# Kernel tuning notes

Measured on AMD Instinct MI355X. Metric: run time of the kernel, lower is better.

The kernel has to match this reference:

```python
import jax, jax.numpy as jnp
import numpy as np

N, D, C = 32768, 1024, 256
GAMMA = 1e-4


def setup_inputs() -> dict:
    key = jax.random.key(0)
    kx, kw = jax.random.split(key)
    X = jax.random.normal(kx, (N, D), dtype=jnp.float32)
    # lcls linear params: weight [C, D], bias [C] (torch nn.Linear layout)
    W = jax.random.normal(kw, (C, D), dtype=jnp.float32) * (1.0 / np.sqrt(D))
    b = jnp.zeros((C,), dtype=jnp.float32)
    return {"X": X, "W": W, "b": b}


def reference(X, W, b):
    # P = softmax(X @ W.T + b) over cluster dim C
    P = jax.nn.softmax(X @ W.T + b, axis=-1)            # [N, C]
    # Reorder P @ P.T @ X -> P @ (P.T @ X): avoids the O(N^2) affinity matrix
    PtX = jnp.einsum('nc,nd->cd', P, X)                  # [C, D]
    return X + GAMMA * (P @ PtX)                         # [N, D]
```

## Files before the change

### kernel.cpp

```cpp
#include <hip/hip_runtime.h>
#include <hip/hip_bf16.h>
#include <stdint.h>

#define N_TOK 32768
#define DIM   1024
#define NC    256
#define GAMMA_F 1e-4f

typedef unsigned short u16;
typedef __attribute__((ext_vector_type(8))) short bf16x8;
typedef __attribute__((ext_vector_type(4))) float f32x4;

__device__ __forceinline__ u16 f2b(float f) {
  union { float f; uint32_t u; } c; c.f = f;
  uint32_t u = c.u;
  return (u16)((u + 0x7FFFu + ((u >> 16) & 1u)) >> 16);
}

__device__ __forceinline__ void gll16(const void* g, void* l) {
  __builtin_amdgcn_global_load_lds(
      (const __attribute__((address_space(1))) unsigned int*)g,
      (__attribute__((address_space(3))) unsigned int*)l, 16, 0, 0);
}


__global__ __launch_bounds__(256) void k0_transpose(const float* __restrict__ X,
                                                    u16* __restrict__ TX) {
  __shared__ u16 tile[64][68];
  const int n0 = blockIdx.x * 64;
  const int d0 = blockIdx.y * 64;
  const int t = threadIdx.x;
  const int r = t >> 4;
  const int c4 = (t & 15) * 4;
#pragma unroll
  for (int i = 0; i < 4; ++i) {
    const int row = r + i * 16;
    const float4 v = *reinterpret_cast<const float4*>(&X[(size_t)(n0 + row) * DIM + d0 + c4]);
    tile[row][c4 + 0] = f2b(v.x);
    tile[row][c4 + 1] = f2b(v.y);
    tile[row][c4 + 2] = f2b(v.z);
    tile[row][c4 + 3] = f2b(v.w);
  }
  __syncthreads();
#pragma unroll
  for (int i = 0; i < 4; ++i) {
    const int drow = r + i * 16;
    ushort4 o;
    o.x = tile[c4 + 0][drow];
    o.y = tile[c4 + 1][drow];
    o.z = tile[c4 + 2][drow];
    o.w = tile[c4 + 3][drow];
    *reinterpret_cast<ushort4*>(&TX[(size_t)(d0 + drow) * N_TOK + n0 + c4]) = o;
  }
}

__global__ __launch_bounds__(256) void k0_convert_w(const float* __restrict__ W,
                                                    u16* __restrict__ Wb) {
  const int idx = (blockIdx.x * 256 + threadIdx.x) * 4;
  const float4 v = *reinterpret_cast<const float4*>(&W[idx]);
  ushort4 o;
  o.x = f2b(v.x); o.y = f2b(v.y); o.z = f2b(v.z); o.w = f2b(v.w);
  *reinterpret_cast<ushort4*>(&Wb[idx]) = o;
}

__global__ __launch_bounds__(256, 2) void p1_fused(const float* __restrict__ X,
                                                   const u16* __restrict__ Wb,
                                                   const float* __restrict__ bias,
                                                   u16* __restrict__ P,
                                                   u16* __restrict__ PT) {
  __shared__ __align__(16) char smem[40960];
  u16* As = (u16*)smem;
  u16* Bs = (u16*)(smem + 8192);
  const int t = threadIdx.x;
  const int lane = t & 63, wave = t >> 6;
  const int wm = wave & 1, wn = wave >> 1;
  const int id = blockIdx.x;
  const int n0 = ((id & 7) * 64 + (id >> 3)) * 64;
  const int frow = lane & 15, fq = lane >> 4;
  const int au = t & 7, ar0 = t >> 3;
  const int bug = (lane & 7) ^ (lane >> 3);

  f32x4 acc[2][8] = {};
  for (int kt = 0; kt < 16; ++kt) {
    const int k0 = kt * 64;
#pragma unroll
    for (int h = 0; h < 2; ++h) {
      const int r = ar0 + h * 32;
      const size_t gb = (size_t)(n0 + r) * DIM + k0 + au * 8;
      const float4 v0 = *reinterpret_cast<const float4*>(&X[gb]);
      const float4 v1 = *reinterpret_cast<const float4*>(&X[gb + 4]);
      bf16x8 u;
      u[0] = (short)f2b(v0.x); u[1] = (short)f2b(v0.y);
      u[2] = (short)f2b(v0.z); u[3] = (short)f2b(v0.w);
      u[4] = (short)f2b(v1.x); u[5] = (short)f2b(v1.y);
      u[6] = (short)f2b(v1.z); u[7] = (short)f2b(v1.w);
      *reinterpret_cast<bf16x8*>(&As[r * 64 + ((au ^ (r & 7)) * 8)]) = u;
    }
#pragma unroll
    for (int i = 0; i < 8; ++i) {
      const int chunk = wave * 8 + i;
      const int brow = chunk * 8 + (lane >> 3);
      gll16(&Wb[(size_t)brow * DIM + k0 + bug * 8], &Bs[chunk * 512]);
    }
    __syncthreads();
#pragma unroll
    for (int ks = 0; ks < 2; ++ks) {
      bf16x8 af[2], bg[8];
#pragma unroll
      for (int m = 0; m < 2; ++m) {
        const int r = wm * 32 + m * 16 + frow;
        af[m] = *reinterpret_cast<const bf16x8*>(&As[r * 64 + (((ks * 4 + fq) ^ (r & 7)) * 8)]);
      }
#pragma unroll
      for (int n = 0; n < 8; ++n) {
        const int r = wn * 128 + n * 16 + frow;
        bg[n] = *reinterpret_cast<const bf16x8*>(&Bs[r * 64 + (((ks * 4 + fq) ^ (r & 7)) * 8)]);
      }
#pragma unroll
      for (int m = 0; m < 2; ++m)
#pragma unroll
        for (int n = 0; n < 8; ++n)
          acc[m][n] = __builtin_amdgcn_mfma_f32_16x16x32_bf16(af[m], bg[n], acc[m][n], 0, 0, 0);
    }
    __syncthreads();
  }

  u16*   Su     = (u16*)smem;
  float* red_mx = (float*)(smem + 33280);
  float* red_sm = (float*)(smem + 33792);

  float bias_r[8];
#pragma unroll
  for (int n = 0; n < 8; ++n) bias_r[n] = bias[wn * 128 + n * 16 + frow];
#pragma unroll
  for (int m = 0; m < 2; ++m)
#pragma unroll
    for (int n = 0; n < 8; ++n)
#pragma unroll
      for (int j = 0; j < 4; ++j) acc[m][n][j] += bias_r[n];

  float mx[2][4];
#pragma unroll
  for (int m = 0; m < 2; ++m)
#pragma unroll
    for (int j = 0; j < 4; ++j) {
      float v = acc[m][0][j];
#pragma unroll
      for (int n = 1; n < 8; ++n) v = fmaxf(v, acc[m][n][j]);
#pragma unroll
      for (int s = 1; s < 16; s <<= 1) v = fmaxf(v, __shfl_xor(v, s, 64));
      mx[m][j] = v;
    }
  if (frow == 0) {
#pragma unroll
    for (int m = 0; m < 2; ++m)
#pragma unroll
      for (int j = 0; j < 4; ++j)
        red_mx[(wm * 32 + m * 16 + fq * 4 + j) * 2 + wn] = mx[m][j];
  }
  __syncthreads();

  const float l2e = 1.44269504088896f;
  float psum[2][4];
#pragma unroll
  for (int m = 0; m < 2; ++m)
#pragma unroll
    for (int j = 0; j < 4; ++j) {
      const int row = wm * 32 + m * 16 + fq * 4 + j;
      const float2 r2 = *reinterpret_cast<const float2*>(&red_mx[row * 2]);
      const float M = fmaxf(r2.x, r2.y);
      float s = 0.f;
#pragma unroll
      for (int n = 0; n < 8; ++n) {
        const float e = exp2f((acc[m][n][j] - M) * l2e);
        acc[m][n][j] = e;
        s += e;
      }
#pragma unroll
      for (int ss = 1; ss < 16; ss <<= 1) s += __shfl_xor(s, ss, 64);
      psum[m][j] = s;
    }
  if (frow == 0) {
#pragma unroll
    for (int m = 0; m < 2; ++m)
#pragma unroll
      for (int j = 0; j < 4; ++j)
        red_sm[(wm * 32 + m * 16 + fq * 4 + j) * 2 + wn] = psum[m][j];
  }
  __syncthreads();

#pragma unroll
  for (int m = 0; m < 2; ++m)
#pragma unroll
    for (int j = 0; j < 4; ++j) {
      const int row = wm * 32 + m * 16 + fq * 4 + j;
      const float2 r2 = *reinterpret_cast<const float2*>(&red_sm[row * 2]);
      const float iv = 1.0f / (r2.x + r2.y);
      const int sw = (row & 7) << 2;
#pragma unroll
      for (int n = 0; n < 8; ++n)
        Su[row * 260 + ((wn * 128 + n * 16 + frow) ^ sw)] = f2b(acc[m][n][j] * iv);
    }
  __syncthreads();

#pragma unroll
  for (int g = 0; g < 16; ++g) {
    const int row = g * 4 + wave;
    const int c = lane * 4;
    const ushort4 v = *reinterpret_cast<const ushort4*>(&Su[row * 260 + (c ^ ((row & 7) << 2))]);
    *reinterpret_cast<ushort4*>(&P[(size_t)(n0 + row) * NC + c]) = v;
  }
#pragma unroll
  for (int it = 0; it < 16; ++it) {
    const int c = it * 16 + wave * 4 + fq;
    const int n = frow * 4;
    ushort4 o;
    o.x = Su[(n + 0) * 260 + (c ^ (((n + 0) & 7) << 2))];
    o.y = Su[(n + 1) * 260 + (c ^ (((n + 1) & 7) << 2))];
    o.z = Su[(n + 2) * 260 + (c ^ (((n + 2) & 7) << 2))];
    o.w = Su[(n + 3) * 260 + (c ^ (((n + 3) & 7) << 2))];
    *reinterpret_cast<ushort4*>(&PT[(size_t)c * N_TOK + n0 + n]) = o;
  }
}

__global__ __launch_bounds__(256, 3) void p2_gemm(const u16* __restrict__ TX,
                                                  const u16* __restrict__ PT,
                                                  float* __restrict__ part) {
  __shared__ __align__(16) char smem[34816];
  u16* As = (u16*)smem;
  u16* Bs = (u16*)(smem + 16384);
  const int t = threadIdx.x;
  const int lane = t & 63, wave = t >> 6;
  const int wm = wave & 1, wn = wave >> 1;
  const int id = blockIdx.x;
  const int swz = (id & 7) * 64 + (id >> 3);
  const int d0 = (swz & 7) * 128;
  const int sk = (swz >> 3) & 31;
  const int c0 = (swz >> 8) * 128;
  const int frow = lane & 15, fq = lane >> 4;
  const int srow = lane >> 3;
  const int bug = (lane & 7) ^ (lane >> 3);
  f32x4 acc[4][4] = {};
  for (int kt = 0; kt < 16; ++kt) {
    const size_t k0 = (size_t)sk * 1024 + kt * 64;
#pragma unroll
    for (int i = 0; i < 4; ++i) {
      const int chunk = wave * 4 + i;
      const int r = chunk * 8 + srow;
      gll16(&TX[(size_t)(d0 + r) * N_TOK + k0 + bug * 8], &As[chunk * 512]);
      gll16(&PT[(size_t)(c0 + r) * N_TOK + k0 + bug * 8], &Bs[chunk * 512]);
    }
    __syncthreads();
#pragma unroll
    for (int ks = 0; ks < 2; ++ks) {
      bf16x8 af[4], bg[4];
#pragma unroll
      for (int m = 0; m < 4; ++m) {
        const int r = wm * 64 + m * 16 + frow;
        af[m] = *reinterpret_cast<const bf16x8*>(&As[r * 64 + (((ks * 4 + fq) ^ (r & 7)) * 8)]);
      }
#pragma unroll
      for (int n = 0; n < 4; ++n) {
        const int r = wn * 64 + n * 16 + frow;
        bg[n] = *reinterpret_cast<const bf16x8*>(&Bs[r * 64 + (((ks * 4 + fq) ^ (r & 7)) * 8)]);
      }
#pragma unroll
      for (int m = 0; m < 4; ++m)
#pragma unroll
        for (int n = 0; n < 4; ++n)
          acc[m][n] = __builtin_amdgcn_mfma_f32_16x16x32_bf16(af[m], bg[n], acc[m][n], 0, 0, 0);
    }
    __syncthreads();
  }
  float* Cf = (float*)smem;
  float* pl = part + (size_t)sk * (DIM * NC);
  const int cl = (t & 31) * 4;
  const int rq = t >> 5;
#pragma unroll
  for (int h = 0; h < 2; ++h) {
    __syncthreads();
    if (wm == h) {
#pragma unroll
      for (int m = 0; m < 4; ++m)
#pragma unroll
        for (int n = 0; n < 4; ++n) {
          const int rr = m * 16 + fq * 4;
          const int col = wn * 64 + n * 16 + frow;
#pragma unroll
          for (int j = 0; j < 4; ++j)
            Cf[(rr + j) * 132 + col] = acc[m][n][j];
        }
    }
    __syncthreads();
#pragma unroll
    for (int p = 0; p < 8; ++p) {
      const int row = p * 8 + rq;
      const float4 v = *reinterpret_cast<const float4*>(&Cf[row * 132 + cl]);
      *reinterpret_cast<float4*>(&pl[(size_t)(d0 + h * 64 + row) * NC + c0 + cl]) = v;
    }
  }
}

__global__ __launch_bounds__(256) void k2_reduce(const float* __restrict__ part,
                                                 u16* __restrict__ PtXb) {
  const int g = (blockIdx.x * 256 + threadIdx.x) * 4;
  f32x4 s = {0.f, 0.f, 0.f, 0.f};
#pragma unroll
  for (int p = 0; p < 32; ++p)
    s += *reinterpret_cast<const f32x4*>(&part[(size_t)p * (DIM * NC) + g]);
  ushort4 o;
  o.x = f2b(s[0] * GAMMA_F); o.y = f2b(s[1] * GAMMA_F);
  o.z = f2b(s[2] * GAMMA_F); o.w = f2b(s[3] * GAMMA_F);
  *reinterpret_cast<ushort4*>(&PtXb[g]) = o;
}

__global__ __launch_bounds__(256, 3) void p3_gemm(const u16* __restrict__ P,
                                                  const u16* __restrict__ PtXb,
                                                  const float* __restrict__ X,
                                                  float* __restrict__ Out) {
  __shared__ __align__(16) char smem[34816];
  u16* As = (u16*)smem;
  u16* Bs = (u16*)(smem + 16384);
  const int t = threadIdx.x;
  const int lane = t & 63, wave = t >> 6;
  const int wm = wave & 1, wn = wave >> 1;
  const int id = blockIdx.x;
  const int swz = (id & 7) * 256 + (id >> 3);
  const int n0 = (swz & 255) * 128;
  const int d0 = (swz >> 8) * 128;
  const int frow = lane & 15, fq = lane >> 4;
  const int srow = lane >> 3;
  const int bug = (lane & 7) ^ (lane >> 3);
  f32x4 acc[4][4] = {};
  for (int kt = 0; kt < 4; ++kt) {
    const int k0 = kt * 64;
#pragma unroll
    for (int i = 0; i < 4; ++i) {
      const int chunk = wave * 4 + i;
      const int r = chunk * 8 + srow;
      gll16(&P[(size_t)(n0 + r) * NC + k0 + bug * 8], &As[chunk * 512]);
      gll16(&PtXb[(size_t)(d0 + r) * NC + k0 + bug * 8], &Bs[chunk * 512]);
    }
    __syncthreads();
#pragma unroll
    for (int ks = 0; ks < 2; ++ks) {
      bf16x8 af[4], bg[4];
#pragma unroll
      for (int m = 0; m < 4; ++m) {
        const int r = wm * 64 + m * 16 + frow;
        af[m] = *reinterpret_cast<const bf16x8*>(&As[r * 64 + (((ks * 4 + fq) ^ (r & 7)) * 8)]);
      }
#pragma unroll
      for (int n = 0; n < 4; ++n) {
        const int r = wn * 64 + n * 16 + frow;
        bg[n] = *reinterpret_cast<const bf16x8*>(&Bs[r * 64 + (((ks * 4 + fq) ^ (r & 7)) * 8)]);
      }
#pragma unroll
      for (int m = 0; m < 4; ++m)
#pragma unroll
        for (int n = 0; n < 4; ++n)
          acc[m][n] = __builtin_amdgcn_mfma_f32_16x16x32_bf16(af[m], bg[n], acc[m][n], 0, 0, 0);
    }
    __syncthreads();
  }
  float* Cf = (float*)smem;
  const int cl = (t & 31) * 4;
  const int rq = t >> 5;
#pragma unroll
  for (int h = 0; h < 2; ++h) {
    __syncthreads();
    if (wm == h) {
#pragma unroll
      for (int m = 0; m < 4; ++m)
#pragma unroll
        for (int n = 0; n < 4; ++n) {
          const int rr = m * 16 + fq * 4;
          const int col = wn * 64 + n * 16 + frow;
#pragma unroll
          for (int j = 0; j < 4; ++j)
            Cf[(rr + j) * 132 + col] = acc[m][n][j];
        }
    }
    __syncthreads();
#pragma unroll
    for (int p = 0; p < 8; ++p) {
      const int row = p * 8 + rq;
      float4 v = *reinterpret_cast<const float4*>(&Cf[row * 132 + cl]);
      const size_t off = (size_t)(n0 + h * 64 + row) * DIM + d0 + cl;
      const float4 x = *reinterpret_cast<const float4*>(&X[off]);
      v.x += x.x; v.y += x.y; v.z += x.z; v.w += x.w;
      *reinterpret_cast<float4*>(&Out[off]) = v;
    }
  }
}

extern "C" void kernel_launch(void* const* d_in, const int* in_sizes, int n_in,
                              void* d_out, int out_size, void* d_ws, size_t ws_size,
                              hipStream_t stream) {
  const float* X = (const float*)d_in[0];
  const float* W = (const float*)d_in[1];
  const float* b = (const float*)d_in[2];
  float* Out = (float*)d_out;
  char* ws = (char*)d_ws;

  const size_t OFF_TX   = 0;
  const size_t OFF_WB   = (size_t)64 << 20;
  const size_t OFF_PTXB = OFF_WB + ((size_t)512 << 10);
  const size_t OFF_PART = (size_t)65 << 20;
  const size_t OFF_P    = (size_t)97 << 20;
  const size_t OFF_PT   = (size_t)113 << 20;
  const size_t NEED     = (size_t)129 << 20;
  if (ws_size < NEED) return;

  u16*   TX   = (u16*)(ws + OFF_TX);
  u16*   Wb   = (u16*)(ws + OFF_WB);
  u16*   PtXb = (u16*)(ws + OFF_PTXB);
  float* part = (float*)(ws + OFF_PART);
  u16*   Pp   = (u16*)(ws + OFF_P);
  u16*   PT   = (u16*)(ws + OFF_PT);

  k0_transpose<<<dim3(N_TOK / 64, DIM / 64), 256, 0, stream>>>(X, TX);
  k0_convert_w<<<dim3((NC * DIM) / 1024), 256, 0, stream>>>(W, Wb);
  p1_fused<<<dim3(N_TOK / 64), 256, 0, stream>>>(X, Wb, b, Pp, PT);
  p2_gemm<<<dim3(512), 256, 0, stream>>>(TX, PT, part);
  k2_reduce<<<dim3((DIM * NC) / 1024), 256, 0, stream>>>(part, PtXb);
  p3_gemm<<<dim3(2048), 256, 0, stream>>>(Pp, PtXb, X, Out);
}
```

Baseline: 387.2 us.

## Fuse X transpose and bf16 conversion into the P^T X GEMM loader

Removes the separate transpose kernel that wrote a bf16 transposed copy of X, and has the P^T X GEMM read fp32 X directly, convert it and store it transposed into LDS. The tiling also changes to 64 D-rows by all 256 clusters per block, so each block covers the full C dimension and reads X only once per split. This avoids a full 128MB read plus 64MB write pass over X, at the cost of scalar fp32 global loads and register-level packing in the GEMM's inner loop instead of async global-to-LDS loads.

```diff
diff --git a/kernel.cpp b/kernel.cpp
--- a/kernel.cpp
+++ b/kernel.cpp
@@ -23,36 +23,6 @@
       (__attribute__((address_space(3))) unsigned int*)l, 16, 0, 0);
 }
 
-
-__global__ __launch_bounds__(256) void k0_transpose(const float* __restrict__ X,
-                                                    u16* __restrict__ TX) {
-  __shared__ u16 tile[64][68];
-  const int n0 = blockIdx.x * 64;
-  const int d0 = blockIdx.y * 64;
-  const int t = threadIdx.x;
-  const int r = t >> 4;
-  const int c4 = (t & 15) * 4;
-#pragma unroll
-  for (int i = 0; i < 4; ++i) {
-    const int row = r + i * 16;
-    const float4 v = *reinterpret_cast<const float4*>(&X[(size_t)(n0 + row) * DIM + d0 + c4]);
-    tile[row][c4 + 0] = f2b(v.x);
-    tile[row][c4 + 1] = f2b(v.y);
-    tile[row][c4 + 2] = f2b(v.z);
-    tile[row][c4 + 3] = f2b(v.w);
-  }
-  __syncthreads();
-#pragma unroll
-  for (int i = 0; i < 4; ++i) {
-    const int drow = r + i * 16;
-    ushort4 o;
-    o.x = tile[c4 + 0][drow];
-    o.y = tile[c4 + 1][drow];
-    o.z = tile[c4 + 2][drow];
-    o.w = tile[c4 + 3][drow];
-    *reinterpret_cast<ushort4*>(&TX[(size_t)(d0 + drow) * N_TOK + n0 + c4]) = o;
-  }
-}
 
 __global__ __launch_bounds__(256) void k0_convert_w(const float* __restrict__ W,
                                                     u16* __restrict__ Wb) {
@@ -223,32 +193,42 @@
   }
 }
 
-__global__ __launch_bounds__(256, 3) void p2_gemm(const u16* __restrict__ TX,
-                                                  const u16* __restrict__ PT,
-                                                  float* __restrict__ part) {
-  __shared__ __align__(16) char smem[34816];
+__global__ __launch_bounds__(256, 3) void p2_direct(const float* __restrict__ X,
+                                                    const u16* __restrict__ PT,
+                                                    float* __restrict__ part) {
+  __shared__ __align__(16) char smem[40960];
   u16* As = (u16*)smem;
-  u16* Bs = (u16*)(smem + 16384);
+  u16* Bs = (u16*)(smem + 8192);
   const int t = threadIdx.x;
   const int lane = t & 63, wave = t >> 6;
-  const int wm = wave & 1, wn = wave >> 1;
   const int id = blockIdx.x;
-  const int swz = (id & 7) * 64 + (id >> 3);
-  const int d0 = (swz & 7) * 128;
-  const int sk = (swz >> 3) & 31;
-  const int c0 = (swz >> 8) * 128;
+  const int wgid = (id & 7) * 64 + (id >> 3);
+  const int d0 = (wgid & 15) * 64;
+  const int sk = wgid >> 4;
   const int frow = lane & 15, fq = lane >> 4;
-  const int srow = lane >> 3;
+  const int dloc = t & 31;
+  const int kp = t >> 5;
   const int bug = (lane & 7) ^ (lane >> 3);
   f32x4 acc[4][4] = {};
   for (int kt = 0; kt < 16; ++kt) {
-    const size_t k0 = (size_t)sk * 1024 + kt * 64;
-#pragma unroll
-    for (int i = 0; i < 4; ++i) {
-      const int chunk = wave * 4 + i;
-      const int r = chunk * 8 + srow;
-      gll16(&TX[(size_t)(d0 + r) * N_TOK + k0 + bug * 8], &As[chunk * 512]);
-      gll16(&PT[(size_t)(c0 + r) * N_TOK + k0 + bug * 8], &Bs[chunk * 512]);
+    const size_t nb = (size_t)sk * 1024 + kt * 64;
+#pragma unroll
+    for (int pass = 0; pass < 4; ++pass) {
+      const int kk = pass * 16 + kp * 2;
+#pragma unroll
+      for (int jj = 0; jj < 2; ++jj) {
+        const int d = dloc + jj * 32;
+        const float x0 = X[(nb + kk) * DIM + d0 + d];
+        const float x1 = X[(nb + kk + 1) * DIM + d0 + d];
+        const uint32_t pk = (uint32_t)f2b(x0) | ((uint32_t)f2b(x1) << 16);
+        *reinterpret_cast<uint32_t*>(&As[d * 64 + (((kk >> 3) ^ (d & 7)) * 8) + (kk & 7)]) = pk;
+      }
+    }
+#pragma unroll
+    for (int i = 0; i < 16; ++i) {
+      const int ch = wave * 16 + i;
+      const int c = ch * 8 + (lane >> 3);
+      gll16(&PT[(size_t)c * N_TOK + nb + bug * 8], &Bs[ch * 512]);
     }
     __syncthreads();
 #pragma unroll
@@ -256,12 +236,12 @@
       bf16x8 af[4], bg[4];
 #pragma unroll
       for (int m = 0; m < 4; ++m) {
-        const int r = wm * 64 + m * 16 + frow;
+        const int r = m * 16 + frow;
         af[m] = *reinterpret_cast<const bf16x8*>(&As[r * 64 + (((ks * 4 + fq) ^ (r & 7)) * 8)]);
       }
 #pragma unroll
       for (int n = 0; n < 4; ++n) {
-        const int r = wn * 64 + n * 16 + frow;
+        const int r = wave * 64 + n * 16 + frow;
         bg[n] = *reinterpret_cast<const bf16x8*>(&Bs[r * 64 + (((ks * 4 + fq) ^ (r & 7)) * 8)]);
       }
 #pragma unroll
@@ -274,29 +254,29 @@
   }
   float* Cf = (float*)smem;
   float* pl = part + (size_t)sk * (DIM * NC);
-  const int cl = (t & 31) * 4;
-  const int rq = t >> 5;
+  const int cl = (t & 63) * 4;
+  const int rr = t >> 6;
 #pragma unroll
   for (int h = 0; h < 2; ++h) {
     __syncthreads();
-    if (wm == h) {
-#pragma unroll
-      for (int m = 0; m < 4; ++m)
-#pragma unroll
-        for (int n = 0; n < 4; ++n) {
-          const int rr = m * 16 + fq * 4;
-          const int col = wn * 64 + n * 16 + frow;
-#pragma unroll
-          for (int j = 0; j < 4; ++j)
-            Cf[(rr + j) * 132 + col] = acc[m][n][j];
-        }
+#pragma unroll
+    for (int mm = 0; mm < 2; ++mm) {
+      const int m = h * 2 + mm;
+#pragma unroll
+      for (int n = 0; n < 4; ++n) {
+        const int rloc = mm * 16 + fq * 4;
+        const int col = wave * 64 + n * 16 + frow;
+#pragma unroll
+        for (int j = 0; j < 4; ++j)
+          Cf[(rloc + j) * 260 + col] = acc[m][n][j];
+      }
     }
     __syncthreads();
 #pragma unroll
     for (int p = 0; p < 8; ++p) {
-      const int row = p * 8 + rq;
-      const float4 v = *reinterpret_cast<const float4*>(&Cf[row * 132 + cl]);
-      *reinterpret_cast<float4*>(&pl[(size_t)(d0 + h * 64 + row) * NC + c0 + cl]) = v;
+      const int row = p * 4 + rr;
+      const f32x4 v = *reinterpret_cast<const f32x4*>(&Cf[row * 260 + cl]);
+      *reinterpret_cast<f32x4*>(&pl[(size_t)(d0 + h * 32 + row) * NC + cl]) = v;
     }
   }
 }
@@ -403,26 +383,23 @@
   float* Out = (float*)d_out;
   char* ws = (char*)d_ws;
 
-  const size_t OFF_TX   = 0;
-  const size_t OFF_WB   = (size_t)64 << 20;
-  const size_t OFF_PTXB = OFF_WB + ((size_t)512 << 10);
-  const size_t OFF_PART = (size_t)65 << 20;
-  const size_t OFF_P    = (size_t)97 << 20;
-  const size_t OFF_PT   = (size_t)113 << 20;
-  const size_t NEED     = (size_t)129 << 20;
+  const size_t OFF_WB   = 0;
+  const size_t OFF_PTXB = (size_t)512 << 10;
+  const size_t OFF_PART = (size_t)1 << 20;
+  const size_t OFF_P    = (size_t)34 << 20;
+  const size_t OFF_PT   = (size_t)50 << 20;
+  const size_t NEED     = (size_t)66 << 20;
   if (ws_size < NEED) return;
 
-  u16*   TX   = (u16*)(ws + OFF_TX);
   u16*   Wb   = (u16*)(ws + OFF_WB);
   u16*   PtXb = (u16*)(ws + OFF_PTXB);
   float* part = (float*)(ws + OFF_PART);
   u16*   Pp   = (u16*)(ws + OFF_P);
   u16*   PT   = (u16*)(ws + OFF_PT);
 
-  k0_transpose<<<dim3(N_TOK / 64, DIM / 64), 256, 0, stream>>>(X, TX);
   k0_convert_w<<<dim3((NC * DIM) / 1024), 256, 0, stream>>>(W, Wb);
   p1_fused<<<dim3(N_TOK / 64), 256, 0, stream>>>(X, Wb, b, Pp, PT);
-  p2_gemm<<<dim3(512), 256, 0, stream>>>(TX, PT, part);
+  p2_direct<<<dim3(512), 256, 0, stream>>>(X, PT, part);
   k2_reduce<<<dim3((DIM * NC) / 1024), 256, 0, stream>>>(part, PtXb);
   p3_gemm<<<dim3(2048), 256, 0, stream>>>(Pp, PtXb, X, Out);
 }
```

After: 354.0 us. -8.6%, faster.
